# Kernel optimization log

Hardware: AMD Instinct MI355X
Metric: run time of the kernel (lower is better)

Reference implementation:

```python
import jax, jax.numpy as jnp
import numpy as np
import math

B, L, C = 1, 4096, 1024
H = 16
D = C // H  # head_dim = 64


def setup_inputs() -> dict:
    key = jax.random.key(0)
    ks = jax.random.split(key, 5)
    s = 1.0 / math.sqrt(C)
    return {
        "x": jax.random.normal(ks[0], (B, L, C), dtype=jnp.float32),
        "Wq": jax.random.normal(ks[1], (C, C), dtype=jnp.float32) * s,
        "Wk": jax.random.normal(ks[2], (C, C), dtype=jnp.float32) * s,
        "Wv": jax.random.normal(ks[3], (C, C), dtype=jnp.float32) * s,
        "Wo": jax.random.normal(ks[4], (C, C), dtype=jnp.float32) * s,
    }


def reference(x, Wq, Wk, Wv, Wo):
    # Projections (bias=False). Wq etc. are applied as x @ W (equivalent
    # parameterization to torch Linear's x @ W.T with transposed storage).
    q = (x @ Wq).reshape(B, L, H, D).transpose(0, 2, 1, 3)  # (B,H,L,D)
    k = (x @ Wk).reshape(B, L, H, D).transpose(0, 2, 1, 3)
    v = (x @ Wv).reshape(B, L, H, D).transpose(0, 2, 1, 3)

    scale = 1.0 / math.sqrt(D)
    scores = jnp.einsum("bhqd,bhkd->bhqk", q, k) * scale  # (B,H,L,L)
    causal = jnp.tril(jnp.ones((L, L), dtype=bool))
    scores = jnp.where(causal[None, None, :, :], scores, -jnp.inf)
    probs = jax.nn.softmax(scores, axis=-1)  # dropout p=0 -> identity

    out = jnp.einsum("bhqk,bhkd->bhqd", probs, v)  # (B,H,L,D)
    out = out.transpose(0, 2, 1, 3).reshape(B, L, C)
    return out @ Wo  # resid dropout p=0 -> identity
```

## Files before the change

kernel.cpp:

```cpp
#include <hip/hip_runtime.h>

#define L_SEQ 4096
#define C_DIM 1024
#define H_NUM 16
#define D_HEAD 64
#define LDQK 2048

typedef __bf16 bf16x8 __attribute__((ext_vector_type(8)));
typedef __bf16 bf16x4 __attribute__((ext_vector_type(4)));
typedef float f32x4 __attribute__((ext_vector_type(4)));
typedef float f32x16 __attribute__((ext_vector_type(16)));
typedef unsigned int u32;
typedef u32 u32x4 __attribute__((ext_vector_type(4)));

#define AS1 __attribute__((address_space(1)))
#define AS3 __attribute__((address_space(3)))

#define SC_LOG2E 0.1803368801111204f

__device__ inline __bf16 f2bf(float f) {
  unsigned u = __builtin_bit_cast(unsigned, f);
  u = (u + 0x7fffu + ((u >> 16) & 1u)) >> 16;
  unsigned short s = (unsigned short)u;
  return __builtin_bit_cast(__bf16, s);
}

__device__ inline void gload_lds16(const __bf16* g, __bf16* l) {
  __builtin_amdgcn_global_load_lds((const AS1 void*)g, (AS3 void*)l, 16, 0, 0);
}

__global__ __launch_bounds__(256) void cvt_f32_bf16(const float* __restrict__ in,
                                                    __bf16* __restrict__ out) {
  int i = (blockIdx.x * 256 + threadIdx.x) * 4;
  float4 v = *(const float4*)(in + i);
  bf16x4 o = {f2bf(v.x), f2bf(v.y), f2bf(v.z), f2bf(v.w)};
  *(bf16x4*)(out + i) = o;
}

__global__ __launch_bounds__(256) void transpose_cvt4(const float* __restrict__ W0,
                                                      const float* __restrict__ W1,
                                                      const float* __restrict__ W2,
                                                      const float* __restrict__ W3,
                                                      __bf16* __restrict__ dst) {
  __shared__ float t[32][33];
  const int z = blockIdx.z;
  const float* W = (z == 0) ? W0 : (z == 1) ? W1 : (z == 2) ? W2 : W3;
  __bf16* Wt = dst + (size_t)z * 1048576;
  const int tx = threadIdx.x, ty = threadIdx.y;
  const int c0 = blockIdx.x * 32, r0 = blockIdx.y * 32;
#pragma unroll
  for (int k = 0; k < 4; ++k)
    t[ty + k * 8][tx] = W[(size_t)(r0 + ty + k * 8) * C_DIM + c0 + tx];
  __syncthreads();
#pragma unroll
  for (int k = 0; k < 4; ++k)
    Wt[(size_t)(c0 + ty + k * 8) * C_DIM + r0 + tx] = f2bf(t[tx][ty + k * 8]);
}

template <bool OUT_BF16>
__global__ __launch_bounds__(256) void gemm_bt(const __bf16* __restrict__ A,
                                               const __bf16* __restrict__ Bt,
                                               void* __restrict__ Cp,
                                               int M, int N, int K,
                                               float cscale, int scale_ncols) {
  __shared__ __bf16 As[128 * 32];
  __shared__ __bf16 Bs[128 * 32];
  const int tid = threadIdx.x;
  const int lane = tid & 63;
  const int wave = tid >> 6;
  const int wm = wave >> 1, wn = wave & 1;
  const int c16 = lane & 15, g4 = lane >> 4;
  const int srow = lane >> 2, scol = (lane & 3) * 8;

  f32x4 acc[4][4] = {};

  const size_t arow0 = (size_t)blockIdx.x * 128;
  const size_t brow0 = (size_t)blockIdx.y * 128;

  for (int kt = 0; kt < K; kt += 32) {
#pragma unroll
    for (int i = 0; i < 2; ++i) {
      const int row = i * 64 + wave * 16 + srow;
      gload_lds16(A + (arow0 + row) * K + kt + scol, As + (i * 64 + wave * 16) * 32);
      gload_lds16(Bt + (brow0 + row) * K + kt + scol, Bs + (i * 64 + wave * 16) * 32);
    }
    __syncthreads();
    bf16x8 af[4], bfr[4];
#pragma unroll
    for (int mi = 0; mi < 4; ++mi)
      af[mi] = *(const bf16x8*)(As + (wm * 64 + mi * 16 + c16) * 32 + g4 * 8);
#pragma unroll
    for (int ni = 0; ni < 4; ++ni)
      bfr[ni] = *(const bf16x8*)(Bs + (wn * 64 + ni * 16 + c16) * 32 + g4 * 8);
#pragma unroll
    for (int mi = 0; mi < 4; ++mi)
#pragma unroll
      for (int ni = 0; ni < 4; ++ni)
        acc[mi][ni] = __builtin_amdgcn_mfma_f32_16x16x32_bf16(af[mi], bfr[ni], acc[mi][ni], 0, 0, 0);
    __syncthreads();
  }

  const float esc = ((int)brow0 < scale_ncols) ? cscale : 1.0f;
#pragma unroll
  for (int mi = 0; mi < 4; ++mi)
#pragma unroll
    for (int ni = 0; ni < 4; ++ni)
#pragma unroll
      for (int i = 0; i < 4; ++i) {
        size_t row = arow0 + wm * 64 + mi * 16 + g4 * 4 + i;
        size_t col = brow0 + wn * 64 + ni * 16 + c16;
        if (OUT_BF16)
          ((__bf16*)Cp)[row * N + col] = f2bf(acc[mi][ni][i] * esc);
        else
          ((float*)Cp)[row * N + col] = acc[mi][ni][i];
      }
}

__global__ __launch_bounds__(256, 2) void attn_fwd(const __bf16* __restrict__ Q,
                                                   const __bf16* __restrict__ Kg,
                                                   const __bf16* __restrict__ Vt,
                                                   __bf16* __restrict__ O) {
  const int bid = blockIdx.x;
  const int h = bid & 15;
  const int g = (bid >> 4) & 15;
  const int qt = (bid < 256) ? (31 - g) : g;
  const int nt = 2 * qt + 2;

  __shared__ __bf16 Ks[2][64 * 64];
  __shared__ __bf16 Vs[2][64 * 64];

  const int tid = threadIdx.x;
  const int lane = tid & 63;
  const int wave = tid >> 6;
  const int l31 = lane & 31;
  const int hl = lane >> 5;
  const int qbase = qt * 128 + wave * 32;
  const int q = qbase + l31;
  const int kvmax_w = (qbase + 31) >> 6;

  const int rl = lane >> 3;
  const int cs = (lane & 7) ^ rl;

  auto stage = [&](int kv, int b) {
#pragma unroll
    for (int i = 0; i < 2; ++i) {
      const int r = (i * 4 + wave) * 8 + rl;
      gload_lds16(Kg + (size_t)(kv * 64 + r) * LDQK + h * D_HEAD + cs * 8,
                  &Ks[b][(i * 4 + wave) * 512]);
      gload_lds16(Vt + (size_t)(h * D_HEAD + r) * L_SEQ + kv * 64 + cs * 8,
                  &Vs[b][(i * 4 + wave) * 512]);
    }
  };

  stage(0, 0);

  bf16x8 qf[4];
  {
    const __bf16* qp = Q + (size_t)q * LDQK + h * D_HEAD + hl * 8;
#pragma unroll
    for (int s = 0; s < 4; ++s) qf[s] = *(const bf16x8*)(qp + s * 16);
  }

  f32x16 acc0 = {}, acc1 = {};
  float m = -1e30f, lsum = 0.f;

  int cur = 0;
  for (int kv = 0; kv < nt; ++kv) {
    if (kv + 1 < nt) {
      stage(kv + 1, cur ^ 1);
      asm volatile("s_waitcnt vmcnt(4)" ::: "memory");
    } else {
      asm volatile("s_waitcnt vmcnt(0)" ::: "memory");
    }
    __builtin_amdgcn_sched_barrier(0);
    __builtin_amdgcn_s_barrier();
    __builtin_amdgcn_sched_barrier(0);

    if (kv <= kvmax_w) {
      char* const KsB = (char*)&Ks[cur][0];
      char* const VsB = (char*)&Vs[cur][0];

      f32x16 st0 = {}, st1 = {};
      __builtin_amdgcn_s_setprio(1);
#pragma unroll
      for (int s = 0; s < 4; ++s) {
        const int ch = s * 2 + hl;
        bf16x8 a0 = *(const bf16x8*)(KsB + l31 * 128 + ((ch ^ (l31 & 7)) << 4));
        bf16x8 a1 = *(const bf16x8*)(KsB + (32 + l31) * 128 + ((ch ^ (l31 & 7)) << 4));
        st0 = __builtin_amdgcn_mfma_f32_32x32x16_bf16(a0, qf[s], st0, 0, 0, 0);
        st1 = __builtin_amdgcn_mfma_f32_32x32x16_bf16(a1, qf[s], st1, 0, 0, 0);
      }
      __builtin_amdgcn_s_setprio(0);

      if (kv == kvmax_w) {
#pragma unroll
        for (int r = 0; r < 16; ++r) {
          const int kr = (r & 3) + 8 * (r >> 2) + 4 * hl;
          const int k0 = kv * 64 + kr;
          st0[r] = (k0 <= q) ? st0[r] : -1e30f;
          st1[r] = (k0 + 32 <= q) ? st1[r] : -1e30f;
        }
      }

      float t[16];
#pragma unroll
      for (int r = 0; r < 16; ++r) t[r] = fmaxf(st0[r], st1[r]);
#pragma unroll
      for (int w = 8; w > 0; w >>= 1)
#pragma unroll
        for (int r = 0; r < w; ++r) t[r] = fmaxf(t[r], t[r + w]);
      float mx = fmaxf(t[0], __shfl_xor(t[0], 32, 64));
      const float mnew = fmaxf(m, mx);
      const float corr = exp2f(m - mnew);
      m = mnew;

#pragma unroll
      for (int r = 0; r < 16; ++r) {
        st0[r] = exp2f(st0[r] - m);
        st1[r] = exp2f(st1[r] - m);
      }
      float sm[16];
#pragma unroll
      for (int r = 0; r < 16; ++r) sm[r] = st0[r] + st1[r];
#pragma unroll
      for (int w = 8; w > 0; w >>= 1)
#pragma unroll
        for (int r = 0; r < w; ++r) sm[r] = sm[r] + sm[r + w];
      float sl = sm[0] + __shfl_xor(sm[0], 32, 64);
      lsum = lsum * corr + sl;
      acc0 *= corr;
      acc1 *= corr;

      u32 w0[8], w1[8];
#pragma unroll
      for (int i = 0; i < 8; ++i) {
        asm("v_cvt_pk_bf16_f32 %0, %1, %2" : "=v"(w0[i]) : "v"(st0[2 * i]), "v"(st0[2 * i + 1]));
        asm("v_cvt_pk_bf16_f32 %0, %1, %2" : "=v"(w1[i]) : "v"(st1[2 * i]), "v"(st1[2 * i + 1]));
      }
      u32 e0a = (u32)__shfl_xor((int)(hl ? w0[0] : w0[2]), 32, 64);
      u32 e0b = (u32)__shfl_xor((int)(hl ? w0[1] : w0[3]), 32, 64);
      u32 e0c = (u32)__shfl_xor((int)(hl ? w0[4] : w0[6]), 32, 64);
      u32 e0d = (u32)__shfl_xor((int)(hl ? w0[5] : w0[7]), 32, 64);
      u32 e1a = (u32)__shfl_xor((int)(hl ? w1[0] : w1[2]), 32, 64);
      u32 e1b = (u32)__shfl_xor((int)(hl ? w1[1] : w1[3]), 32, 64);
      u32 e1c = (u32)__shfl_xor((int)(hl ? w1[4] : w1[6]), 32, 64);
      u32 e1d = (u32)__shfl_xor((int)(hl ? w1[5] : w1[7]), 32, 64);
      u32x4 f0 = hl ? (u32x4){e0a, e0b, w0[2], w0[3]} : (u32x4){w0[0], w0[1], e0a, e0b};
      u32x4 f1 = hl ? (u32x4){e0c, e0d, w0[6], w0[7]} : (u32x4){w0[4], w0[5], e0c, e0d};
      u32x4 f2 = hl ? (u32x4){e1a, e1b, w1[2], w1[3]} : (u32x4){w1[0], w1[1], e1a, e1b};
      u32x4 f3 = hl ? (u32x4){e1c, e1d, w1[6], w1[7]} : (u32x4){w1[4], w1[5], e1c, e1d};
      bf16x8 pb0 = __builtin_bit_cast(bf16x8, f0);
      bf16x8 pb1 = __builtin_bit_cast(bf16x8, f1);
      bf16x8 pb2 = __builtin_bit_cast(bf16x8, f2);
      bf16x8 pb3 = __builtin_bit_cast(bf16x8, f3);

      __builtin_amdgcn_s_setprio(1);
#pragma unroll
      for (int s = 0; s < 4; ++s) {
        const bf16x8 pb = (s == 0) ? pb0 : (s == 1) ? pb1 : (s == 2) ? pb2 : pb3;
        const int ch = s * 2 + hl;
        bf16x8 va0 = *(const bf16x8*)(VsB + l31 * 128 + ((ch ^ (l31 & 7)) << 4));
        bf16x8 va1 = *(const bf16x8*)(VsB + (32 + l31) * 128 + ((ch ^ (l31 & 7)) << 4));
        acc0 = __builtin_amdgcn_mfma_f32_32x32x16_bf16(va0, pb, acc0, 0, 0, 0);
        acc1 = __builtin_amdgcn_mfma_f32_32x32x16_bf16(va1, pb, acc1, 0, 0, 0);
      }
      __builtin_amdgcn_s_setprio(0);
    }

    __builtin_amdgcn_sched_barrier(0);
    __builtin_amdgcn_s_barrier();
    __builtin_amdgcn_sched_barrier(0);
    cur ^= 1;
  }

  const float rinv = 1.0f / lsum;
  char* const Po = (char*)&Ks[0][0] + wave * 4096;
#pragma unroll
  for (int dt = 0; dt < 2; ++dt) {
#pragma unroll
    for (int i = 0; i < 8; ++i) {
      const int r = 2 * i;
      const int d = dt * 32 + (r & 3) + 8 * (r >> 2) + 4 * hl;
      float lo = (dt ? acc1[r] : acc0[r]) * rinv;
      float hi = (dt ? acc1[r + 1] : acc0[r + 1]) * rinv;
      u32 wv;
      asm("v_cvt_pk_bf16_f32 %0, %1, %2" : "=v"(wv) : "v"(lo), "v"(hi));
      *(u32*)(Po + l31 * 128 + (((d >> 3) ^ (l31 & 7)) << 4) + (d & 7) * 2) = wv;
    }
  }
  asm volatile("s_waitcnt lgkmcnt(0)" ::: "memory");
  __builtin_amdgcn_sched_barrier(0);
#pragma unroll
  for (int j = 0; j < 4; ++j) {
    const int qr = lane >> 1;
    const int c = (lane & 1) * 4 + j;
    bf16x8 ov = *(const bf16x8*)(Po + qr * 128 + ((c ^ (qr & 7)) << 4));
    *(bf16x8*)(O + (size_t)(qbase + qr) * C_DIM + h * D_HEAD + c * 8) = ov;
  }
}

extern "C" void kernel_launch(void* const* d_in, const int* in_sizes, int n_in,
                              void* d_out, int out_size, void* d_ws, size_t ws_size,
                              hipStream_t stream) {
  const float* x = (const float*)d_in[0];
  const float* Wq = (const float*)d_in[1];
  const float* Wk = (const float*)d_in[2];
  const float* Wv = (const float*)d_in[3];
  const float* Wo = (const float*)d_in[4];
  float* out = (float*)d_out;

  char* ws = (char*)d_ws;
  __bf16* xb    = (__bf16*)(ws);
  __bf16* WqkvT = (__bf16*)(ws + (8u << 20));
  __bf16* QKb   = (__bf16*)(ws + (16u << 20));
  __bf16* Vtb   = (__bf16*)(ws + (32u << 20));
  __bf16* WvT   = WqkvT + (size_t)2 * 1048576;
  __bf16* WoT   = WqkvT + (size_t)3 * 1048576;
  __bf16* Ab    = xb;

  cvt_f32_bf16<<<4096, 256, 0, stream>>>(x, xb);

  transpose_cvt4<<<dim3(32, 32, 4), dim3(32, 8), 0, stream>>>(Wq, Wk, Wv, Wo, WqkvT);

  gemm_bt<true><<<dim3(32, 16), 256, 0, stream>>>(
      xb, WqkvT, QKb, L_SEQ, LDQK, C_DIM, SC_LOG2E, 1024);

  gemm_bt<true><<<dim3(8, 32), 256, 0, stream>>>(
      WvT, xb, Vtb, C_DIM, L_SEQ, C_DIM, 1.0f, 0);

  attn_fwd<<<512, 256, 0, stream>>>(QKb, QKb + 1024, Vtb, Ab);

  gemm_bt<false><<<dim3(32, 8), 256, 0, stream>>>(
      Ab, WoT, out, L_SEQ, C_DIM, C_DIM, 1.0f, 0);
}
```

Before: 278.1 us.

## Merge prep kernels, fuse QKV GEMMs, pair causal tiles per attention block

```diff
diff --git a/kernel.cpp b/kernel.cpp
--- a/kernel.cpp
+++ b/kernel.cpp
@@ -29,32 +29,107 @@
   __builtin_amdgcn_global_load_lds((const AS1 void*)g, (AS3 void*)l, 16, 0, 0);
 }
 
-__global__ __launch_bounds__(256) void cvt_f32_bf16(const float* __restrict__ in,
-                                                    __bf16* __restrict__ out) {
-  int i = (blockIdx.x * 256 + threadIdx.x) * 4;
-  float4 v = *(const float4*)(in + i);
-  bf16x4 o = {f2bf(v.x), f2bf(v.y), f2bf(v.z), f2bf(v.w)};
-  *(bf16x4*)(out + i) = o;
-}
-
-__global__ __launch_bounds__(256) void transpose_cvt4(const float* __restrict__ W0,
-                                                      const float* __restrict__ W1,
-                                                      const float* __restrict__ W2,
-                                                      const float* __restrict__ W3,
-                                                      __bf16* __restrict__ dst) {
+__global__ __launch_bounds__(256) void prep(const float* __restrict__ x,
+                                            const float* __restrict__ W0,
+                                            const float* __restrict__ W1,
+                                            const float* __restrict__ W2,
+                                            const float* __restrict__ W3,
+                                            __bf16* __restrict__ xb,
+                                            __bf16* __restrict__ Wt) {
   __shared__ float t[32][33];
-  const int z = blockIdx.z;
+  int id = blockIdx.x;
+  if (id < 4096) {
+    int i = (id * 256 + threadIdx.x) * 4;
+    float4 v = *(const float4*)(x + i);
+    bf16x4 o = {f2bf(v.x), f2bf(v.y), f2bf(v.z), f2bf(v.w)};
+    *(bf16x4*)(xb + i) = o;
+    return;
+  }
+  id -= 4096;
+  const int z = id >> 10;
+  const int rem = id & 1023;
   const float* W = (z == 0) ? W0 : (z == 1) ? W1 : (z == 2) ? W2 : W3;
-  __bf16* Wt = dst + (size_t)z * 1048576;
-  const int tx = threadIdx.x, ty = threadIdx.y;
-  const int c0 = blockIdx.x * 32, r0 = blockIdx.y * 32;
+  __bf16* dst = Wt + (size_t)z * 1048576;
+  const int tx = threadIdx.x & 31, ty = threadIdx.x >> 5;
+  const int c0 = (rem & 31) * 32, r0 = (rem >> 5) * 32;
 #pragma unroll
   for (int k = 0; k < 4; ++k)
     t[ty + k * 8][tx] = W[(size_t)(r0 + ty + k * 8) * C_DIM + c0 + tx];
   __syncthreads();
 #pragma unroll
   for (int k = 0; k < 4; ++k)
-    Wt[(size_t)(c0 + ty + k * 8) * C_DIM + r0 + tx] = f2bf(t[tx][ty + k * 8]);
+    dst[(size_t)(c0 + ty + k * 8) * C_DIM + r0 + tx] = f2bf(t[tx][ty + k * 8]);
+}
+
+__global__ __launch_bounds__(256) void gemm_qkv(const __bf16* __restrict__ xb,
+                                                const __bf16* __restrict__ WqkT,
+                                                const __bf16* __restrict__ WvT,
+                                                __bf16* __restrict__ QKb,
+                                                __bf16* __restrict__ Vtb) {
+  __shared__ __bf16 As[128 * 32];
+  __shared__ __bf16 Bs[128 * 32];
+  int g = blockIdx.x;
+  const __bf16 *A, *Bt;
+  __bf16* C;
+  int N;
+  size_t arow0, brow0;
+  float esc;
+  if (g < 512) {
+    A = xb; Bt = WqkT; C = QKb; N = 2048;
+    arow0 = (size_t)(g & 31) * 128;
+    brow0 = (size_t)(g >> 5) * 128;
+    esc = ((int)brow0 < 1024) ? SC_LOG2E : 1.0f;
+  } else {
+    g -= 512;
+    A = WvT; Bt = xb; C = Vtb; N = 4096;
+    arow0 = (size_t)(g & 7) * 128;
+    brow0 = (size_t)(g >> 3) * 128;
+    esc = 1.0f;
+  }
+  const int K = 1024;
+
+  const int tid = threadIdx.x;
+  const int lane = tid & 63;
+  const int wave = tid >> 6;
+  const int wm = wave >> 1, wn = wave & 1;
+  const int c16 = lane & 15, g4 = lane >> 4;
+  const int srow = lane >> 2, scol = (lane & 3) * 8;
+
+  f32x4 acc[4][4] = {};
+
+  for (int kt = 0; kt < K; kt += 32) {
+#pragma unroll
+    for (int i = 0; i < 2; ++i) {
+      const int row = i * 64 + wave * 16 + srow;
+      gload_lds16(A + (arow0 + row) * K + kt + scol, As + (i * 64 + wave * 16) * 32);
+      gload_lds16(Bt + (brow0 + row) * K + kt + scol, Bs + (i * 64 + wave * 16) * 32);
+    }
+    __syncthreads();
+    bf16x8 af[4], bfr[4];
+#pragma unroll
+    for (int mi = 0; mi < 4; ++mi)
+      af[mi] = *(const bf16x8*)(As + (wm * 64 + mi * 16 + c16) * 32 + g4 * 8);
+#pragma unroll
+    for (int ni = 0; ni < 4; ++ni)
+      bfr[ni] = *(const bf16x8*)(Bs + (wn * 64 + ni * 16 + c16) * 32 + g4 * 8);
+#pragma unroll
+    for (int mi = 0; mi < 4; ++mi)
+#pragma unroll
+      for (int ni = 0; ni < 4; ++ni)
+        acc[mi][ni] = __builtin_amdgcn_mfma_f32_16x16x32_bf16(af[mi], bfr[ni], acc[mi][ni], 0, 0, 0);
+    __syncthreads();
+  }
+
+#pragma unroll
+  for (int mi = 0; mi < 4; ++mi)
+#pragma unroll
+    for (int ni = 0; ni < 4; ++ni)
+#pragma unroll
+      for (int i = 0; i < 4; ++i) {
+        size_t row = arow0 + wm * 64 + mi * 16 + g4 * 4 + i;
+        size_t col = brow0 + wn * 64 + ni * 16 + c16;
+        C[row * N + col] = f2bf(acc[mi][ni][i] * esc);
+      }
 }
 
 template <bool OUT_BF16>
@@ -116,32 +191,31 @@
       }
 }
 
-__global__ __launch_bounds__(256, 2) void attn_fwd(const __bf16* __restrict__ Q,
+__global__ __launch_bounds__(256, 1) void attn_fwd(const __bf16* __restrict__ Q,
                                                    const __bf16* __restrict__ Kg,
                                                    const __bf16* __restrict__ Vt,
                                                    __bf16* __restrict__ O) {
   const int bid = blockIdx.x;
   const int h = bid & 15;
-  const int g = (bid >> 4) & 15;
-  const int qt = (bid < 256) ? (31 - g) : g;
-  const int nt = 2 * qt + 2;
-
-  __shared__ __bf16 Ks[2][64 * 64];
-  __shared__ __bf16 Vs[2][64 * 64];
+  const int p = bid >> 4;
+  const int qtA = 31 - p, qtB = p;
+  const int ntA = 2 * qtA + 2;
+  const int NT = 66;
+
+  __shared__ __bf16 Ks[3][64 * 64];
+  __shared__ __bf16 Vs[3][64 * 64];
+  __shared__ __bf16 PoS[4][2048];
 
   const int tid = threadIdx.x;
   const int lane = tid & 63;
   const int wave = tid >> 6;
   const int l31 = lane & 31;
   const int hl = lane >> 5;
-  const int qbase = qt * 128 + wave * 32;
-  const int q = qbase + l31;
-  const int kvmax_w = (qbase + 31) >> 6;
-
   const int rl = lane >> 3;
   const int cs = (lane & 7) ^ rl;
 
-  auto stage = [&](int kv, int b) {
+  auto stage = [&](int idx, int b) {
+    const int kv = (idx < ntA) ? idx : idx - ntA;
 #pragma unroll
     for (int i = 0; i < 2; ++i) {
       const int r = (i * 4 + wave) * 8 + rl;
@@ -152,33 +226,75 @@
     }
   };
 
+  int qbase = qtA * 128 + wave * 32;
+  bf16x8 qf[4], qfB[4];
+  {
+    const __bf16* qp = Q + (size_t)(qbase + l31) * LDQK + h * D_HEAD + hl * 8;
+#pragma unroll
+    for (int s = 0; s < 4; ++s) qf[s] = *(const bf16x8*)(qp + s * 16);
+    const __bf16* qp2 = Q + (size_t)(qtB * 128 + wave * 32 + l31) * LDQK + h * D_HEAD + hl * 8;
+#pragma unroll
+    for (int s = 0; s < 4; ++s) qfB[s] = *(const bf16x8*)(qp2 + s * 16);
+  }
+
   stage(0, 0);
-
-  bf16x8 qf[4];
-  {
-    const __bf16* qp = Q + (size_t)q * LDQK + h * D_HEAD + hl * 8;
-#pragma unroll
-    for (int s = 0; s < 4; ++s) qf[s] = *(const bf16x8*)(qp + s * 16);
-  }
+  stage(1, 1);
+
+  int kvmax_w = 2 * qtA + (wave >> 1);
+  int q = qbase + l31;
 
   f32x16 acc0 = {}, acc1 = {};
   float m = -1e30f, lsum = 0.f;
-
-  int cur = 0;
-  for (int kv = 0; kv < nt; ++kv) {
-    if (kv + 1 < nt) {
-      stage(kv + 1, cur ^ 1);
+  int bc = 0;
+
+  auto epilogue = [&]() {
+    const float rinv = 1.0f / lsum;
+    char* const Po = (char*)&PoS[wave][0];
+#pragma unroll
+    for (int dt = 0; dt < 2; ++dt) {
+#pragma unroll
+      for (int i = 0; i < 8; ++i) {
+        const int r = 2 * i;
+        const int d = dt * 32 + (r & 3) + 8 * (r >> 2) + 4 * hl;
+        float lo = (dt ? acc1[r] : acc0[r]) * rinv;
+        float hi = (dt ? acc1[r + 1] : acc0[r + 1]) * rinv;
+        u32 wv;
+        asm("v_cvt_pk_bf16_f32 %0, %1, %2" : "=v"(wv) : "v"(lo), "v"(hi));
+        *(u32*)(Po + l31 * 128 + (((d >> 3) ^ (l31 & 7)) << 4) + (d & 7) * 2) = wv;
+      }
+    }
+    asm volatile("s_waitcnt lgkmcnt(0)" ::: "memory");
+    __builtin_amdgcn_sched_barrier(0);
+#pragma unroll
+    for (int j = 0; j < 4; ++j) {
+      const int qr = lane >> 1;
+      const int c = (lane & 1) * 4 + j;
+      bf16x8 ov = *(const bf16x8*)(Po + qr * 128 + ((c ^ (qr & 7)) << 4));
+      *(bf16x8*)(O + (size_t)(qbase + qr) * C_DIM + h * D_HEAD + c * 8) = ov;
+    }
+  };
+
+  for (int idx = 0; idx < NT; ++idx) {
+    __builtin_amdgcn_sched_barrier(0);
+    __builtin_amdgcn_s_barrier();
+    __builtin_amdgcn_sched_barrier(0);
+
+    if (idx + 2 < NT) {
+      int bs = bc + 2; if (bs >= 3) bs -= 3;
+      stage(idx + 2, bs);
+      asm volatile("s_waitcnt vmcnt(8)" ::: "memory");
+    } else if (idx + 2 == NT) {
       asm volatile("s_waitcnt vmcnt(4)" ::: "memory");
     } else {
       asm volatile("s_waitcnt vmcnt(0)" ::: "memory");
     }
     __builtin_amdgcn_sched_barrier(0);
-    __builtin_amdgcn_s_barrier();
-    __builtin_amdgcn_sched_barrier(0);
-
-    if (kv <= kvmax_w) {
-      char* const KsB = (char*)&Ks[cur][0];
-      char* const VsB = (char*)&Vs[cur][0];
+
+    const int kvl = (idx < ntA) ? idx : idx - ntA;
+
+    if (kvl <= kvmax_w) {
+      char* const KsB = (char*)&Ks[bc][0];
+      char* const VsB = (char*)&Vs[bc][0];
 
       f32x16 st0 = {}, st1 = {};
       __builtin_amdgcn_s_setprio(1);
@@ -192,11 +308,11 @@
       }
       __builtin_amdgcn_s_setprio(0);
 
-      if (kv == kvmax_w) {
+      if (kvl == kvmax_w) {
 #pragma unroll
         for (int r = 0; r < 16; ++r) {
           const int kr = (r & 3) + 8 * (r >> 2) + 4 * hl;
-          const int k0 = kv * 64 + kr;
+          const int k0 = kvl * 64 + kr;
           st0[r] = (k0 <= q) ? st0[r] : -1e30f;
           st1[r] = (k0 + 32 <= q) ? st1[r] : -1e30f;
         }
@@ -267,36 +383,23 @@
       __builtin_amdgcn_s_setprio(0);
     }
 
-    __builtin_amdgcn_sched_barrier(0);
-    __builtin_amdgcn_s_barrier();
-    __builtin_amdgcn_sched_barrier(0);
-    cur ^= 1;
-  }
-
-  const float rinv = 1.0f / lsum;
-  char* const Po = (char*)&Ks[0][0] + wave * 4096;
-#pragma unroll
-  for (int dt = 0; dt < 2; ++dt) {
-#pragma unroll
-    for (int i = 0; i < 8; ++i) {
-      const int r = 2 * i;
-      const int d = dt * 32 + (r & 3) + 8 * (r >> 2) + 4 * hl;
-      float lo = (dt ? acc1[r] : acc0[r]) * rinv;
-      float hi = (dt ? acc1[r + 1] : acc0[r + 1]) * rinv;
-      u32 wv;
-      asm("v_cvt_pk_bf16_f32 %0, %1, %2" : "=v"(wv) : "v"(lo), "v"(hi));
-      *(u32*)(Po + l31 * 128 + (((d >> 3) ^ (l31 & 7)) << 4) + (d & 7) * 2) = wv;
-    }
-  }
-  asm volatile("s_waitcnt lgkmcnt(0)" ::: "memory");
-  __builtin_amdgcn_sched_barrier(0);
-#pragma unroll
-  for (int j = 0; j < 4; ++j) {
-    const int qr = lane >> 1;
-    const int c = (lane & 1) * 4 + j;
-    bf16x8 ov = *(const bf16x8*)(Po + qr * 128 + ((c ^ (qr & 7)) << 4));
-    *(bf16x8*)(O + (size_t)(qbase + qr) * C_DIM + h * D_HEAD + c * 8) = ov;
-  }
+    if (idx == ntA - 1) {
+      epilogue();
+      qbase = qtB * 128 + wave * 32;
+      q = qbase + l31;
+      kvmax_w = 2 * qtB + (wave >> 1);
+#pragma unroll
+      for (int s = 0; s < 4; ++s) qf[s] = qfB[s];
+      acc0 = (f32x16){};
+      acc1 = (f32x16){};
+      m = -1e30f;
+      lsum = 0.f;
+    }
+
+    bc = (bc + 1 == 3) ? 0 : bc + 1;
+  }
+
+  epilogue();
 }
 
 extern "C" void kernel_launch(void* const* d_in, const int* in_sizes, int n_in,
@@ -318,17 +421,11 @@
   __bf16* WoT   = WqkvT + (size_t)3 * 1048576;
   __bf16* Ab    = xb;
 
-  cvt_f32_bf16<<<4096, 256, 0, stream>>>(x, xb);
-
-  transpose_cvt4<<<dim3(32, 32, 4), dim3(32, 8), 0, stream>>>(Wq, Wk, Wv, Wo, WqkvT);
-
-  gemm_bt<true><<<dim3(32, 16), 256, 0, stream>>>(
-      xb, WqkvT, QKb, L_SEQ, LDQK, C_DIM, SC_LOG2E, 1024);
-
-  gemm_bt<true><<<dim3(8, 32), 256, 0, stream>>>(
-      WvT, xb, Vtb, C_DIM, L_SEQ, C_DIM, 1.0f, 0);
-
-  attn_fwd<<<512, 256, 0, stream>>>(QKb, QKb + 1024, Vtb, Ab);
+  prep<<<8192, 256, 0, stream>>>(x, Wq, Wk, Wv, Wo, xb, WqkvT);
+
+  gemm_qkv<<<768, 256, 0, stream>>>(xb, WqkvT, WvT, QKb, Vtb);
+
+  attn_fwd<<<256, 256, 0, stream>>>(QKb, QKb + 1024, Vtb, Ab);
 
   gemm_bt<false><<<dim3(32, 8), 256, 0, stream>>>(
       Ab, WoT, out, L_SEQ, C_DIM, C_DIM, 1.0f, 0);
```

Result: no change. 275.3 us (-1.0%).
